# Kernel tuning notes

Measured on AMD Instinct MI355X. Metric: run time of the kernel, lower is better.

## Reference

```python
import jax, jax.numpy as jnp
import numpy as np

N_NODES = 10000
N_EDGES = 640000
N_GRAPHS = 64
D = 128
N_BLOCKS = 2
NEG_SLOPE = 0.01  # F.leaky_relu default


def setup_inputs() -> dict:
    key = jax.random.key(0)
    ks = jax.random.split(key, 9)
    x = jax.random.normal(ks[0], (N_NODES, D), dtype=jnp.float32)
    edge_src = jax.random.randint(ks[1], (N_EDGES,), 0, N_NODES, dtype=jnp.int32)
    edge_dst = jax.random.randint(ks[2], (N_EDGES,), 0, N_NODES, dtype=jnp.int32)
    graph_ids = jnp.sort(jax.random.randint(ks[3], (N_NODES,), 0, N_GRAPHS, dtype=jnp.int32))
    s = 1.414 / np.sqrt(D)  # xavier-normal-ish scale
    Wfc = jax.random.normal(ks[4], (N_BLOCKS, D, D), dtype=jnp.float32) * s
    bfc = jnp.zeros((N_BLOCKS, D), dtype=jnp.float32)
    wl = jax.random.normal(ks[5], (N_BLOCKS, D), dtype=jnp.float32) * s
    wr = jax.random.normal(ks[6], (N_BLOCKS, D), dtype=jnp.float32) * s
    Wres = jax.random.normal(ks[7], (N_BLOCKS, D, D), dtype=jnp.float32) * s
    return {"x": x, "edge_src": edge_src, "edge_dst": edge_dst, "graph_ids": graph_ids,
            "Wfc": Wfc, "bfc": bfc, "wl": wl, "wr": wr, "Wres": Wres}


def _gat_block(x, edge_src, edge_dst, Wfc_b, bfc_b, wl_b, wr_b, Wres_b):
    # node projections: nn.Linear -> x @ W^T + b
    feat = x @ Wfc_b.T + bfc_b                       # [N, D]
    a_self = feat @ wl_b                              # [N] self_a (dst side)
    a_nb = feat @ wr_b                                # [N] attn  (src side)
    # per-edge score: leaky_relu(self_a[dst] + attn[src])
    s = a_self[edge_dst] + a_nb[edge_src]             # [E]
    s = jnp.where(s >= 0, s, NEG_SLOPE * s)
    # segment softmax over incoming edges of each dst node
    m = jax.ops.segment_max(s, edge_dst, num_segments=N_NODES)   # [N]
    e = jnp.exp(s - m[edge_dst])                                  # [E]
    denom = jax.ops.segment_sum(e, edge_dst, num_segments=N_NODES)
    w = e / denom[edge_dst]                                       # [E]
    # attention-weighted neighbor aggregation
    accum = jax.ops.segment_sum(w[:, None] * feat[edge_src], edge_dst,
                                num_segments=N_NODES)             # [N, D]
    # residual (in_size == out_size -> res_fc, no bias), then relu
    out = accum + x @ Wres_b.T
    return jax.nn.relu(out)


def reference(x, edge_src, edge_dst, graph_ids, Wfc, bfc, wl, wr, Wres):
    blocks = [
        _gat_block(x, edge_src, edge_dst, Wfc[b], bfc[b], wl[b], wr[b], Wres[b])
        for b in range(N_BLOCKS)
    ]
    h = jnp.concatenate(blocks, axis=1)               # mode='concat' -> [N, 2*D]
    # dgl.sum_nodes: per-graph sum pooling
    phis = jax.ops.segment_sum(h, graph_ids, num_segments=N_GRAPHS)  # [G, 2*D]
    return h, phis
```

## Files before the change

### kernel.cpp

```cpp
#include <hip/hip_runtime.h>
#include <hip/hip_bf16.h>
#include <math.h>

#define N_NODES 10000
#define N_EDGES 640000
#define N_GRAPHS 64
#define DIM 128
#define NEG_SLOPE 0.01f
#define NB_CSR 128
#define EDGES_PER_BLK (N_EDGES / NB_CSR)


__device__ __forceinline__ unsigned short f2bf(float f) {
    __hip_bfloat16 h = __float2bfloat16(f);
    return *reinterpret_cast<unsigned short*>(&h);
}

typedef __attribute__((ext_vector_type(8))) short short8v;
typedef __attribute__((ext_vector_type(4))) float f32x4;

__global__ __launch_bounds__(512) void csr_hist(const int4* __restrict__ edst4,
                                                int* __restrict__ bh) {
    __shared__ int hist[N_NODES];
    const int blk = blockIdx.x;
    const int t = threadIdx.x;
    for (int n = t; n < N_NODES; n += 512) hist[n] = 0;
    __syncthreads();
    const int base4 = blk * (EDGES_PER_BLK / 4);
    for (int i = t; i < EDGES_PER_BLK / 4; i += 512) {
        int4 d = edst4[base4 + i];
        atomicAdd(&hist[d.x], 1);
        atomicAdd(&hist[d.y], 1);
        atomicAdd(&hist[d.z], 1);
        atomicAdd(&hist[d.w], 1);
    }
    __syncthreads();
    int* dst = bh + (size_t)blk * N_NODES;
    for (int n = t; n < N_NODES; n += 512) dst[n] = hist[n];
}

__global__ __launch_bounds__(256) void csr_node_scan(int* __restrict__ bh,
                                                     int* __restrict__ deg) {
    int n = blockIdx.x * 256 + threadIdx.x;
    if (n >= N_NODES) return;
    int running = 0;
    for (int blk = 0; blk < NB_CSR; ++blk) {
        int* p = bh + (size_t)blk * N_NODES + n;
        int v = *p;
        *p = running;
        running += v;
    }
    deg[n] = running;
}

__global__ __launch_bounds__(1024) void scan_deg(const int* __restrict__ deg,
                                                 int* __restrict__ rowptr) {
    __shared__ int sdata[1024];
    const int tid = threadIdx.x;
    const int base = tid * 10;
    int cnt = N_NODES - base;
    if (cnt < 0) cnt = 0;
    if (cnt > 10) cnt = 10;
    int local[10];
    int s = 0;
    for (int i = 0; i < cnt; ++i) { local[i] = s; s += deg[base + i]; }
    sdata[tid] = s;
    __syncthreads();
    for (int off = 1; off < 1024; off <<= 1) {
        int v = 0;
        if (tid >= off) v = sdata[tid - off];
        __syncthreads();
        if (tid >= off) sdata[tid] += v;
        __syncthreads();
    }
    int pre = (tid == 0) ? 0 : sdata[tid - 1];
    for (int i = 0; i < cnt; ++i) rowptr[base + i] = pre + local[i];
    if (tid == 1023) rowptr[N_NODES] = sdata[1023];
}

__global__ __launch_bounds__(512) void csr_scatter(
    const int4* __restrict__ esrc4, const int4* __restrict__ edst4,
    const int* __restrict__ rowptr, const int* __restrict__ bh,
    int* __restrict__ csr_src) {
    __shared__ int cur[N_NODES];
    const int blk = blockIdx.x;
    const int t = threadIdx.x;
    const int* boff = bh + (size_t)blk * N_NODES;
    for (int n = t; n < N_NODES; n += 512) cur[n] = rowptr[n] + boff[n];
    __syncthreads();
    const int base4 = blk * (EDGES_PER_BLK / 4);
    for (int i = t; i < EDGES_PER_BLK / 4; i += 512) {
        int4 s = esrc4[base4 + i];
        int4 d = edst4[base4 + i];
        csr_src[atomicAdd(&cur[d.x], 1)] = s.x;
        csr_src[atomicAdd(&cur[d.y], 1)] = s.y;
        csr_src[atomicAdd(&cur[d.z], 1)] = s.z;
        csr_src[atomicAdd(&cur[d.w], 1)] = s.w;
    }
}

#define LDK 136
__global__ __launch_bounds__(256) void gemm_mfma(
    const float* __restrict__ x, const float* __restrict__ Wfc,
    const float* __restrict__ bfc, const float* __restrict__ Wres,
    float* __restrict__ resid, unsigned short* __restrict__ feat_b16) {
    __shared__ unsigned short xs[64 * LDK];
    __shared__ unsigned short wsh[128 * LDK];
    const int which = blockIdx.y & 1;
    const int b = blockIdx.y >> 1;
    const float* __restrict__ W = (which ? Wres : Wfc) + (size_t)b * DIM * DIM;
    const int n0 = blockIdx.x * 64;
    const int t = threadIdx.x;

    {
        const int r = t >> 2;
        const int kq = (t & 3) * 32;
        const int n = n0 + r;
        unsigned short tmp[32];
        if (n < N_NODES) {
            const float4* px = reinterpret_cast<const float4*>(x + (size_t)n * DIM + kq);
#pragma unroll
            for (int i = 0; i < 8; ++i) {
                float4 v = px[i];
                tmp[4 * i]     = f2bf(v.x);
                tmp[4 * i + 1] = f2bf(v.y);
                tmp[4 * i + 2] = f2bf(v.z);
                tmp[4 * i + 3] = f2bf(v.w);
            }
        } else {
#pragma unroll
            for (int i = 0; i < 32; ++i) tmp[i] = 0;
        }
#pragma unroll
        for (int i = 0; i < 4; ++i)
            *reinterpret_cast<short8v*>(&xs[r * LDK + kq + 8 * i]) =
                *reinterpret_cast<const short8v*>(&tmp[8 * i]);
    }
    {
        const int r = t >> 1;
        const int kh = (t & 1) * 64;
        const float4* pw = reinterpret_cast<const float4*>(W + (size_t)r * DIM + kh);
        unsigned short tmp[64];
#pragma unroll
        for (int i = 0; i < 16; ++i) {
            float4 v = pw[i];
            tmp[4 * i]     = f2bf(v.x);
            tmp[4 * i + 1] = f2bf(v.y);
            tmp[4 * i + 2] = f2bf(v.z);
            tmp[4 * i + 3] = f2bf(v.w);
        }
#pragma unroll
        for (int i = 0; i < 8; ++i)
            *reinterpret_cast<short8v*>(&wsh[r * LDK + kh + 8 * i]) =
                *reinterpret_cast<const short8v*>(&tmp[8 * i]);
    }
    __syncthreads();

    const int wave = t >> 6;
    const int lane = t & 63;
    const int l16 = lane & 15;
    const int l4 = lane >> 4;

    f32x4 acc[8];
#pragma unroll
    for (int nf = 0; nf < 8; ++nf) acc[nf] = (f32x4){0.f, 0.f, 0.f, 0.f};

    const int arow = wave * 16 + l16;
#pragma unroll
    for (int ks = 0; ks < 4; ++ks) {
        short8v af = *reinterpret_cast<const short8v*>(
            &xs[arow * LDK + ks * 32 + l4 * 8]);
#pragma unroll
        for (int nf = 0; nf < 8; ++nf) {
            short8v bfr = *reinterpret_cast<const short8v*>(
                &wsh[(nf * 16 + l16) * LDK + ks * 32 + l4 * 8]);
            acc[nf] = __builtin_amdgcn_mfma_f32_16x16x32_bf16(af, bfr, acc[nf], 0, 0, 0);
        }
    }

    const int rbase = n0 + wave * 16 + l4 * 4;
    if (which == 0) {
#pragma unroll
        for (int nf = 0; nf < 8; ++nf) {
            const float bias = bfc[b * DIM + nf * 16 + l16];
            unsigned short* dst = feat_b16 + (size_t)b * N_NODES * DIM + nf * 16 + l16;
#pragma unroll
            for (int r = 0; r < 4; ++r) {
                int n = rbase + r;
                if (n < N_NODES) dst[(size_t)n * DIM] = f2bf(acc[nf][r] + bias);
            }
        }
    } else {
        float* dst0 = resid + (size_t)b * N_NODES * DIM;
#pragma unroll
        for (int nf = 0; nf < 8; ++nf) {
#pragma unroll
            for (int r = 0; r < 4; ++r) {
                int n = rbase + r;
                if (n < N_NODES) dst0[(size_t)n * DIM + nf * 16 + l16] = acc[nf][r];
            }
        }
    }
}

__global__ __launch_bounds__(256) void attn_vec(
    const float* __restrict__ x, const float* __restrict__ Wfc,
    const float* __restrict__ bfc,
    const float* __restrict__ wl, const float* __restrict__ wr,
    float* __restrict__ a_self, float* __restrict__ a_nb) {
    __shared__ float u[2][2][DIM];
    __shared__ float c[2][2];
    const int t = threadIdx.x;
    for (int o = t; o < 512; o += 256) {
        int k = o & 127;
        int bb = (o >> 7) & 1;
        int v = o >> 8;
        const float* wv = (v ? wr : wl) + bb * DIM;
        const float* Wb = Wfc + (size_t)bb * DIM * DIM;
        float s = 0.f;
#pragma unroll 4
        for (int j = 0; j < DIM; ++j) s += wv[j] * Wb[j * DIM + k];
        u[v][bb][k] = s;
    }
    if (t < 4) {
        int v = t >> 1, bb = t & 1;
        const float* wv = (v ? wr : wl) + bb * DIM;
        const float* bias = bfc + bb * DIM;
        float s = 0.f;
        for (int j = 0; j < DIM; ++j) s += wv[j] * bias[j];
        c[v][bb] = s;
    }
    __syncthreads();
    int n = blockIdx.x * 256 + t;
    if (n >= N_NODES) return;
    const float4* px = reinterpret_cast<const float4*>(x + (size_t)n * DIM);
    float s00 = 0.f, s01 = 0.f, s10 = 0.f, s11 = 0.f;
#pragma unroll 8
    for (int i = 0; i < 32; ++i) {
        float4 v = px[i];
        const float* u00 = &u[0][0][4 * i];
        const float* u01 = &u[0][1][4 * i];
        const float* u10 = &u[1][0][4 * i];
        const float* u11 = &u[1][1][4 * i];
        s00 += v.x * u00[0] + v.y * u00[1] + v.z * u00[2] + v.w * u00[3];
        s01 += v.x * u01[0] + v.y * u01[1] + v.z * u01[2] + v.w * u01[3];
        s10 += v.x * u10[0] + v.y * u10[1] + v.z * u10[2] + v.w * u10[3];
        s11 += v.x * u11[0] + v.y * u11[1] + v.z * u11[2] + v.w * u11[3];
    }
    a_self[n] = s00 + c[0][0];
    a_self[N_NODES + n] = s01 + c[0][1];
    a_nb[n] = s10 + c[1][0];
    a_nb[N_NODES + n] = s11 + c[1][1];
}

__global__ __launch_bounds__(256) void aggregate(
    const unsigned short* __restrict__ feat_b16, const float* __restrict__ resid,
    const float* __restrict__ a_self, const float* __restrict__ a_nb,
    const int* __restrict__ rowptr, const int* __restrict__ csr_src,
    float* __restrict__ out) {
    const int wave = threadIdx.x >> 6;
    const int lane = threadIdx.x & 63;
    const int n = blockIdx.x * 4 + wave;
    const int b = blockIdx.y;
    const int q = lane >> 4;
    const int l16 = lane & 15;
    const int start = rowptr[n];
    const int end = rowptr[n + 1];

    const float* __restrict__ anb = a_nb + b * N_NODES;
    const uint4* __restrict__ fb =
        reinterpret_cast<const uint4*>(feat_b16 + (size_t)b * N_NODES * DIM);
    const float asl = a_self[b * N_NODES + n];

    float acc[8];
#pragma unroll
    for (int k = 0; k < 8; ++k) acc[k] = 0.f;
    float dpart = 0.f;

    for (int c = start; c < end; c += 64) {
        int j = c + lane;
        float e = 0.f;
        int src = 0;
        if (j < end) {
            src = csr_src[j];
            float s = asl + anb[src];
            s = (s >= 0.f) ? s : NEG_SLOPE * s;
            e = __expf(s);
        }
        dpart += e;
        int cnt = end - c;
        if (cnt > 64) cnt = 64;
        int iters = (cnt + 3) >> 2;

        float w0 = __shfl(e, q, 64);
        int s0 = __shfl(src, q, 64);
        uint4 f0 = fb[(size_t)s0 * 16 + l16];

        for (int i2 = 0; i2 < iters - 1; ++i2) {
            int idx = (i2 + 1) * 4 + q;
            float w1 = __shfl(e, idx, 64);
            int s1 = __shfl(src, idx, 64);
            uint4 f1 = fb[(size_t)s1 * 16 + l16];
#pragma unroll
            for (int k = 0; k < 4; ++k) {
                unsigned int u = (&f0.x)[k];
                float lo = __uint_as_float(u << 16);
                float hi = __uint_as_float(u & 0xffff0000u);
                acc[2 * k]     += w0 * lo;
                acc[2 * k + 1] += w0 * hi;
            }
            w0 = w1; f0 = f1;
        }
#pragma unroll
        for (int k = 0; k < 4; ++k) {
            unsigned int u = (&f0.x)[k];
            float lo = __uint_as_float(u << 16);
            float hi = __uint_as_float(u & 0xffff0000u);
            acc[2 * k]     += w0 * lo;
            acc[2 * k + 1] += w0 * hi;
        }
    }

#pragma unroll
    for (int k = 0; k < 8; ++k) {
        acc[k] += __shfl_xor(acc[k], 16, 64);
        acc[k] += __shfl_xor(acc[k], 32, 64);
    }
    float denom = dpart;
#pragma unroll
    for (int off = 32; off > 0; off >>= 1) denom += __shfl_xor(denom, off, 64);

    if (q == 0) {
        float inv = (end > start) ? 1.f / denom : 0.f;
        const float4* rr = reinterpret_cast<const float4*>(
            resid + ((size_t)b * N_NODES + n) * DIM);
        float4 r0 = rr[l16 * 2];
        float4 r1 = rr[l16 * 2 + 1];
        float4 o0, o1;
        o0.x = fmaxf(acc[0] * inv + r0.x, 0.f);
        o0.y = fmaxf(acc[1] * inv + r0.y, 0.f);
        o0.z = fmaxf(acc[2] * inv + r0.z, 0.f);
        o0.w = fmaxf(acc[3] * inv + r0.w, 0.f);
        o1.x = fmaxf(acc[4] * inv + r1.x, 0.f);
        o1.y = fmaxf(acc[5] * inv + r1.y, 0.f);
        o1.z = fmaxf(acc[6] * inv + r1.z, 0.f);
        o1.w = fmaxf(acc[7] * inv + r1.w, 0.f);
        float4* po = reinterpret_cast<float4*>(out + (size_t)n * (2 * DIM) + b * DIM);
        po[l16 * 2] = o0;
        po[l16 * 2 + 1] = o1;
    }
}

__device__ int lower_bound_dev(const int* __restrict__ a, int n, int key) {
    int lo = 0, hi = n;
    while (lo < hi) {
        int mid = (lo + hi) >> 1;
        if (a[mid] < key) lo = mid + 1;
        else hi = mid;
    }
    return lo;
}

__global__ __launch_bounds__(256) void pool_graphs(
    const float* __restrict__ h, const int* __restrict__ gids,
    float* __restrict__ phis) {
    const int g = blockIdx.x;
    const int chunk = blockIdx.y;
    const int tid = threadIdx.x;
    int lo = lower_bound_dev(gids, N_NODES, g);
    int hi = lower_bound_dev(gids, N_NODES, g + 1);
    float acc = 0.f;
    for (int n = lo + chunk; n < hi; n += 16) acc += h[(size_t)n * (2 * DIM) + tid];
    if (acc != 0.f) atomicAdd(&phis[(size_t)g * (2 * DIM) + tid], acc);
}

extern "C" void kernel_launch(void* const* d_in, const int* in_sizes, int n_in,
                              void* d_out, int out_size, void* d_ws, size_t ws_size,
                              hipStream_t stream) {
    const float* x    = (const float*)d_in[0];
    const int* esrc   = (const int*)d_in[1];
    const int* edst   = (const int*)d_in[2];
    const int* gids   = (const int*)d_in[3];
    const float* Wfc  = (const float*)d_in[4];
    const float* bfc  = (const float*)d_in[5];
    const float* wl   = (const float*)d_in[6];
    const float* wr   = (const float*)d_in[7];
    const float* Wres = (const float*)d_in[8];
    float* out = (float*)d_out;

    char* ws = (char*)d_ws;
    float* resid   = (float*)(ws + 10240000);
    float* a_self  = (float*)(ws + 20480000);
    float* a_nb    = (float*)(ws + 20560000);
    int*   deg     = (int*)(ws + 20640000);
    int*   rowptr  = (int*)(ws + 20688000);
    int*   csr_src = (int*)(ws + 20784000);
    unsigned short* feat_b16 = (unsigned short*)(ws + 23344000);
    int*   bh      = (int*)(ws + 28464000);

    float* phis = out + (size_t)N_NODES * 2 * DIM;

    hipMemsetAsync(phis, 0, N_GRAPHS * 2 * DIM * sizeof(float), stream);

    attn_vec<<<(N_NODES + 255) / 256, 256, 0, stream>>>(
        x, Wfc, bfc, wl, wr, a_self, a_nb);

    csr_hist<<<NB_CSR, 512, 0, stream>>>((const int4*)edst, bh);
    csr_node_scan<<<(N_NODES + 255) / 256, 256, 0, stream>>>(bh, deg);
    scan_deg<<<1, 1024, 0, stream>>>(deg, rowptr);
    csr_scatter<<<NB_CSR, 512, 0, stream>>>(
        (const int4*)esrc, (const int4*)edst, rowptr, bh, csr_src);

    gemm_mfma<<<dim3((N_NODES + 63) / 64, 4), 256, 0, stream>>>(
        x, Wfc, bfc, Wres, resid, feat_b16);

    aggregate<<<dim3(2500, 2), 256, 0, stream>>>(
        feat_b16, resid, a_self, a_nb, rowptr, csr_src, out);
    pool_graphs<<<dim3(N_GRAPHS, 16), 256, 0, stream>>>(out, gids, phis);
}
```

Baseline: 178.6 us.

## Fuse attention vectors into GEMM epilogue and stage outputs through shared memory

The separate attn_vec kernel is removed. The a_self and a_nb dot products are now computed in the fc GEMM epilogue from the fp32 feat values, reduced with wave shuffles. GEMM outputs are staged through a shared-memory tile that reuses the input buffers via a union, so global stores become coalesced vector writes instead of strided scalar ones. csr_node_scan now loads a 128x128 tile of per-block histograms into LDS so the per-node prefix is computed there rather than by serial dependent global read-modify-writes. The attention scores are now computed from unrounded fp32 feat instead of via the precomposed W^T w vector, which changes rounding slightly.

```diff
diff --git a/kernel.cpp b/kernel.cpp
--- a/kernel.cpp
+++ b/kernel.cpp
@@ -39,18 +39,29 @@
     for (int n = t; n < N_NODES; n += 512) dst[n] = hist[n];
 }
 
-__global__ __launch_bounds__(256) void csr_node_scan(int* __restrict__ bh,
+__global__ __launch_bounds__(128) void csr_node_scan(int* __restrict__ bh,
                                                      int* __restrict__ deg) {
-    int n = blockIdx.x * 256 + threadIdx.x;
-    if (n >= N_NODES) return;
-    int running = 0;
-    for (int blk = 0; blk < NB_CSR; ++blk) {
-        int* p = bh + (size_t)blk * N_NODES + n;
-        int v = *p;
-        *p = running;
-        running += v;
-    }
-    deg[n] = running;
+    __shared__ int tile[NB_CSR][128];
+    const int tid = threadIdx.x;
+    const int n = blockIdx.x * 128 + tid;
+    const bool ok = (n < N_NODES);
+#pragma unroll 8
+    for (int r = 0; r < NB_CSR; ++r)
+        tile[r][tid] = ok ? bh[(size_t)r * N_NODES + n] : 0;
+    __syncthreads();
+    int run = 0;
+#pragma unroll 8
+    for (int r = 0; r < NB_CSR; ++r) {
+        int v = tile[r][tid];
+        tile[r][tid] = run;
+        run += v;
+    }
+    if (ok) {
+        deg[n] = run;
+#pragma unroll 8
+        for (int r = 0; r < NB_CSR; ++r)
+            bh[(size_t)r * N_NODES + n] = tile[r][tid];
+    }
 }
 
 __global__ __launch_bounds__(1024) void scan_deg(const int* __restrict__ deg,
@@ -100,12 +111,23 @@
 }
 
 #define LDK 136
+struct GemmSmem {
+    union {
+        struct {
+            unsigned short xs[64 * LDK];
+            unsigned short wsh[128 * LDK];
+        } in;
+        float ot[64 * 132];
+    };
+};
+
 __global__ __launch_bounds__(256) void gemm_mfma(
     const float* __restrict__ x, const float* __restrict__ Wfc,
     const float* __restrict__ bfc, const float* __restrict__ Wres,
-    float* __restrict__ resid, unsigned short* __restrict__ feat_b16) {
-    __shared__ unsigned short xs[64 * LDK];
-    __shared__ unsigned short wsh[128 * LDK];
+    float* __restrict__ resid, unsigned short* __restrict__ feat_b16,
+    const float* __restrict__ wl, const float* __restrict__ wr,
+    float* __restrict__ a_self, float* __restrict__ a_nb) {
+    __shared__ GemmSmem sm;
     const int which = blockIdx.y & 1;
     const int b = blockIdx.y >> 1;
     const float* __restrict__ W = (which ? Wres : Wfc) + (size_t)b * DIM * DIM;
@@ -133,7 +155,7 @@
         }
 #pragma unroll
         for (int i = 0; i < 4; ++i)
-            *reinterpret_cast<short8v*>(&xs[r * LDK + kq + 8 * i]) =
+            *reinterpret_cast<short8v*>(&sm.in.xs[r * LDK + kq + 8 * i]) =
                 *reinterpret_cast<const short8v*>(&tmp[8 * i]);
     }
     {
@@ -151,7 +173,7 @@
         }
 #pragma unroll
         for (int i = 0; i < 8; ++i)
-            *reinterpret_cast<short8v*>(&wsh[r * LDK + kh + 8 * i]) =
+            *reinterpret_cast<short8v*>(&sm.in.wsh[r * LDK + kh + 8 * i]) =
                 *reinterpret_cast<const short8v*>(&tmp[8 * i]);
     }
     __syncthreads();
@@ -169,88 +191,83 @@
 #pragma unroll
     for (int ks = 0; ks < 4; ++ks) {
         short8v af = *reinterpret_cast<const short8v*>(
-            &xs[arow * LDK + ks * 32 + l4 * 8]);
+            &sm.in.xs[arow * LDK + ks * 32 + l4 * 8]);
 #pragma unroll
         for (int nf = 0; nf < 8; ++nf) {
             short8v bfr = *reinterpret_cast<const short8v*>(
-                &wsh[(nf * 16 + l16) * LDK + ks * 32 + l4 * 8]);
+                &sm.in.wsh[(nf * 16 + l16) * LDK + ks * 32 + l4 * 8]);
             acc[nf] = __builtin_amdgcn_mfma_f32_16x16x32_bf16(af, bfr, acc[nf], 0, 0, 0);
         }
     }
 
-    const int rbase = n0 + wave * 16 + l4 * 4;
+    __syncthreads();
+    const int lrow = wave * 16 + l4 * 4;
+
     if (which == 0) {
+        float wlv[8], wrv[8], bv[8];
 #pragma unroll
         for (int nf = 0; nf < 8; ++nf) {
-            const float bias = bfc[b * DIM + nf * 16 + l16];
-            unsigned short* dst = feat_b16 + (size_t)b * N_NODES * DIM + nf * 16 + l16;
-#pragma unroll
-            for (int r = 0; r < 4; ++r) {
-                int n = rbase + r;
-                if (n < N_NODES) dst[(size_t)n * DIM] = f2bf(acc[nf][r] + bias);
+            wlv[nf] = wl[b * DIM + nf * 16 + l16];
+            wrv[nf] = wr[b * DIM + nf * 16 + l16];
+            bv[nf]  = bfc[b * DIM + nf * 16 + l16];
+        }
+#pragma unroll
+        for (int r = 0; r < 4; ++r) {
+            float ps = 0.f, pr = 0.f;
+#pragma unroll
+            for (int nf = 0; nf < 8; ++nf) {
+                float f = acc[nf][r] + bv[nf];
+                sm.ot[(lrow + r) * 132 + nf * 16 + l16] = f;
+                ps += f * wlv[nf];
+                pr += f * wrv[nf];
+            }
+#pragma unroll
+            for (int off = 1; off < 16; off <<= 1) {
+                ps += __shfl_xor(ps, off, 64);
+                pr += __shfl_xor(pr, off, 64);
+            }
+            int n = n0 + lrow + r;
+            if (l16 == 0 && n < N_NODES) {
+                a_self[b * N_NODES + n] = ps;
+                a_nb[b * N_NODES + n] = pr;
             }
         }
     } else {
-        float* dst0 = resid + (size_t)b * N_NODES * DIM;
-#pragma unroll
-        for (int nf = 0; nf < 8; ++nf) {
-#pragma unroll
-            for (int r = 0; r < 4; ++r) {
-                int n = rbase + r;
-                if (n < N_NODES) dst0[(size_t)n * DIM + nf * 16 + l16] = acc[nf][r];
-            }
-        }
-    }
-}
-
-__global__ __launch_bounds__(256) void attn_vec(
-    const float* __restrict__ x, const float* __restrict__ Wfc,
-    const float* __restrict__ bfc,
-    const float* __restrict__ wl, const float* __restrict__ wr,
-    float* __restrict__ a_self, float* __restrict__ a_nb) {
-    __shared__ float u[2][2][DIM];
-    __shared__ float c[2][2];
-    const int t = threadIdx.x;
-    for (int o = t; o < 512; o += 256) {
-        int k = o & 127;
-        int bb = (o >> 7) & 1;
-        int v = o >> 8;
-        const float* wv = (v ? wr : wl) + bb * DIM;
-        const float* Wb = Wfc + (size_t)bb * DIM * DIM;
-        float s = 0.f;
-#pragma unroll 4
-        for (int j = 0; j < DIM; ++j) s += wv[j] * Wb[j * DIM + k];
-        u[v][bb][k] = s;
-    }
-    if (t < 4) {
-        int v = t >> 1, bb = t & 1;
-        const float* wv = (v ? wr : wl) + bb * DIM;
-        const float* bias = bfc + bb * DIM;
-        float s = 0.f;
-        for (int j = 0; j < DIM; ++j) s += wv[j] * bias[j];
-        c[v][bb] = s;
-    }
-    __syncthreads();
-    int n = blockIdx.x * 256 + t;
-    if (n >= N_NODES) return;
-    const float4* px = reinterpret_cast<const float4*>(x + (size_t)n * DIM);
-    float s00 = 0.f, s01 = 0.f, s10 = 0.f, s11 = 0.f;
-#pragma unroll 8
-    for (int i = 0; i < 32; ++i) {
-        float4 v = px[i];
-        const float* u00 = &u[0][0][4 * i];
-        const float* u01 = &u[0][1][4 * i];
-        const float* u10 = &u[1][0][4 * i];
-        const float* u11 = &u[1][1][4 * i];
-        s00 += v.x * u00[0] + v.y * u00[1] + v.z * u00[2] + v.w * u00[3];
-        s01 += v.x * u01[0] + v.y * u01[1] + v.z * u01[2] + v.w * u01[3];
-        s10 += v.x * u10[0] + v.y * u10[1] + v.z * u10[2] + v.w * u10[3];
-        s11 += v.x * u11[0] + v.y * u11[1] + v.z * u11[2] + v.w * u11[3];
-    }
-    a_self[n] = s00 + c[0][0];
-    a_self[N_NODES + n] = s01 + c[0][1];
-    a_nb[n] = s10 + c[1][0];
-    a_nb[N_NODES + n] = s11 + c[1][1];
+#pragma unroll
+        for (int r = 0; r < 4; ++r)
+#pragma unroll
+            for (int nf = 0; nf < 8; ++nf)
+                sm.ot[(lrow + r) * 132 + nf * 16 + l16] = acc[nf][r];
+    }
+    __syncthreads();
+
+    const int rr = t >> 2;
+    const int cq = (t & 3) * 32;
+    const int n = n0 + rr;
+    if (n < N_NODES) {
+        if (which == 0) {
+            unsigned short tmp[32];
+#pragma unroll
+            for (int i = 0; i < 8; ++i) {
+                float4 v = *reinterpret_cast<const float4*>(&sm.ot[rr * 132 + cq + 4 * i]);
+                tmp[4 * i]     = f2bf(v.x);
+                tmp[4 * i + 1] = f2bf(v.y);
+                tmp[4 * i + 2] = f2bf(v.z);
+                tmp[4 * i + 3] = f2bf(v.w);
+            }
+            unsigned short* dst = feat_b16 + ((size_t)b * N_NODES + n) * DIM + cq;
+#pragma unroll
+            for (int i = 0; i < 4; ++i)
+                *reinterpret_cast<short8v*>(dst + 8 * i) =
+                    *reinterpret_cast<const short8v*>(&tmp[8 * i]);
+        } else {
+            float* dst = resid + ((size_t)b * N_NODES + n) * DIM + cq;
+#pragma unroll
+            for (int i = 0; i < 8; ++i)
+                *reinterpret_cast<float4*>(dst + 4 * i) =
+                    *reinterpret_cast<const float4*>(&sm.ot[rr * 132 + cq + 4 * i]);
+        }
+    }
 }
 
 __global__ __launch_bounds__(256) void aggregate(
@@ -402,18 +419,15 @@
 
     hipMemsetAsync(phis, 0, N_GRAPHS * 2 * DIM * sizeof(float), stream);
 
-    attn_vec<<<(N_NODES + 255) / 256, 256, 0, stream>>>(
-        x, Wfc, bfc, wl, wr, a_self, a_nb);
+    gemm_mfma<<<dim3((N_NODES + 63) / 64, 4), 256, 0, stream>>>(
+        x, Wfc, bfc, Wres, resid, feat_b16, wl, wr, a_self, a_nb);
 
     csr_hist<<<NB_CSR, 512, 0, stream>>>((const int4*)edst, bh);
-    csr_node_scan<<<(N_NODES + 255) / 256, 256, 0, stream>>>(bh, deg);
+    csr_node_scan<<<(N_NODES + 127) / 128, 128, 0, stream>>>(bh, deg);
     scan_deg<<<1, 1024, 0, stream>>>(deg, rowptr);
     csr_scatter<<<NB_CSR, 512, 0, stream>>>(
         (const int4*)esrc, (const int4*)edst, rowptr, bh, csr_src);
 
-    gemm_mfma<<<dim3((N_NODES + 63) / 64, 4), 256, 0, stream>>>(
-        x, Wfc, bfc, Wres, resid, feat_b16);
-
     aggregate<<<dim3(2500, 2), 256, 0, stream>>>(
         feat_b16, resid, a_self, a_nb, rowptr, csr_src, out);
     pool_graphs<<<dim3(N_GRAPHS, 16), 256, 0, stream>>>(out, gids, phis);
```

Result: slower. 192.2 us (+7.6%).
